# Kernel optimization log

Hardware: AMD Instinct MI355X
Metric: run time of the kernel (lower is better)

## Reference

```python
import jax, jax.numpy as jnp
import numpy as np

L, C, F, K = 8192, 2048, 128, 257  # timesteps, input_size, filter_size, lag (odd => symmetric 'same' pad)
NY = 256  # number of overwritten channel rows


def setup_inputs() -> dict:
    key = jax.random.key(0)
    k1, k2, k3, k4 = jax.random.split(key, 4)
    x = jax.random.normal(k1, (L, C), dtype=jnp.float32)
    Yt = jax.random.randint(k2, (NY,), 0, C)
    # learned parameters (torch.rand -> uniform[0,1))
    g = jax.random.uniform(k3, (C, F), dtype=jnp.float32)
    kernel = jax.random.uniform(k4, (F, K), dtype=jnp.float32)
    return {"x": x, "Yt": Yt, "g": g, "kernel": kernel}


def reference(x, Yt, g, kernel):
    # synapse[c] is the per-channel 1D filter; the original builds a dense
    # (C, C, K) kernel whose only non-zero slices are the diagonal, so the
    # full conv1d is mathematically a depthwise (grouped) conv.
    synapse = jnp.matmul(g, kernel)          # (C, K)
    lhs = x.T[None]                          # (1, C, L)  NCH
    rhs = synapse[:, None, :]                # (C, 1, K)  OIH, groups=C
    pad = (kernel.shape[1] - 1) // 2         # torch padding='same', odd K
    out = jax.lax.conv_general_dilated(
        lhs, rhs,
        window_strides=(1,),
        padding=[(pad, pad)],
        feature_group_count=x.shape[1],
        dimension_numbers=("NCH", "OIH", "NCH"),
    )                                        # (1, C, L)
    # result[:, Yt, :] = x.T[Yt] : scatter-overwrite selected channel rows
    out = out.at[:, Yt, :].set(x.T[Yt][None])
    return out
```

## Files before the change

kernel.cpp:

```cpp
#include <hip/hip_runtime.h>

#define LL   8192
#define CC   2048
#define FF   128
#define KK   257
#define PAD  128

#define SROW 320
#define NT   18

#define ROWS 1288
#define SRP  328

typedef __bf16 bf16x8 __attribute__((ext_vector_type(8)));
typedef float  f32x16 __attribute__((ext_vector_type(16)));

static __device__ __forceinline__ unsigned short f2bf(float f) {
    unsigned u = __float_as_uint(f);
    u = (u + 0x7fffu + ((u >> 16) & 1u)) >> 16;
    return (unsigned short)u;
}

__global__ __launch_bounds__(256) void synb_kernel(const float* __restrict__ g,
                                                   const float* __restrict__ kern,
                                                   const int* __restrict__ Yt, int ny,
                                                   unsigned short* __restrict__ synEb) {
    __shared__ int sfl[4];
    const int c0 = blockIdx.x * 4;
    const int t  = threadIdx.x;
    if (t < 4) sfl[t] = 0;
    __syncthreads();
    for (int i = t; i < ny; i += 256) {
        int y = Yt[i];
        #pragma unroll
        for (int ii = 0; ii < 4; ++ii) if (y == c0 + ii) sfl[ii] = 1;
    }
    __syncthreads();
    const float* g0 = g + (size_t)(c0 + 0) * FF;
    const float* g1 = g + (size_t)(c0 + 1) * FF;
    const float* g2 = g + (size_t)(c0 + 2) * FF;
    const float* g3 = g + (size_t)(c0 + 3) * FF;
    const int fl0 = sfl[0], fl1 = sfl[1], fl2 = sfl[2], fl3 = sfl[3];
    for (int p = t; p < SROW; p += 256) {
        const int kk = p - 32;
        float a0 = 0.f, a1 = 0.f, a2 = 0.f, a3 = 0.f;
        const bool inr = (kk >= 0) && (kk < KK);
        if (inr) {
            #pragma unroll 8
            for (int f = 0; f < FF; ++f) {
                float kv = kern[f * KK + kk];
                a0 += kv * g0[f];
                a1 += kv * g1[f];
                a2 += kv * g2[f];
                a3 += kv * g3[f];
            }
        }
        float dlt = (kk == PAD) ? 1.f : 0.f;
        float v0 = inr ? (fl0 ? dlt : a0) : 0.f;
        float v1 = inr ? (fl1 ? dlt : a1) : 0.f;
        float v2 = inr ? (fl2 ? dlt : a2) : 0.f;
        float v3 = inr ? (fl3 ? dlt : a3) : 0.f;
        synEb[(size_t)(c0 + 0) * SROW + p] = f2bf(v0);
        synEb[(size_t)(c0 + 1) * SROW + p] = f2bf(v1);
        synEb[(size_t)(c0 + 2) * SROW + p] = f2bf(v2);
        synEb[(size_t)(c0 + 3) * SROW + p] = f2bf(v3);
    }
}

__global__ __launch_bounds__(256) void fused_conv(const float* __restrict__ x,
                                                  const unsigned short* __restrict__ synEb,
                                                  float* __restrict__ out) {
    __shared__ alignas(16) unsigned short xch[16][ROWS];
    __shared__ alignas(16) unsigned short synL[16][SRP];
    const int t  = threadIdx.x;
    const int W0 = blockIdx.x << 10;
    const int c0 = blockIdx.y << 4;

    {
        const int rw = t >> 4;
        const int u  = t & 15;
        const unsigned* src = (const unsigned*)(synEb + (size_t)(c0 + rw) * SROW);
        unsigned* dst = (unsigned*)(synL[rw]);
        #pragma unroll
        for (int k = 0; k < 10; ++k) dst[u + (k << 4)] = src[u + (k << 4)];
    }

    #pragma unroll
    for (int k = 0; k < 10; ++k) {
        int pidx = (k << 8) + t;
        int ch4  = pidx & 3;
        int pp   = pidx >> 2;
        int lg   = W0 + (pp << 1) - 128;
        const float* sp = x + (size_t)lg * CC + c0 + (ch4 << 2);
        float4 ve = make_float4(0.f, 0.f, 0.f, 0.f);
        float4 vo = make_float4(0.f, 0.f, 0.f, 0.f);
        if ((unsigned)lg       < (unsigned)LL) ve = *(const float4*)sp;
        if ((unsigned)(lg + 1) < (unsigned)LL) vo = *(const float4*)(sp + CC);
        int gq = pp >> 2;
        int gp = gq ^ ((gq >> 3) & 7);
        int dw = (gp << 2) | (pp & 3);
        const float* pe = (const float*)&ve;
        const float* po = (const float*)&vo;
        #pragma unroll
        for (int c2 = 0; c2 < 4; ++c2) {
            unsigned val = (unsigned)f2bf(pe[c2]) | ((unsigned)f2bf(po[c2]) << 16);
            ((unsigned*)xch[(ch4 << 2) + c2])[dw] = val;
        }
    }
    __syncthreads();

    const int w = t >> 6, ln = t & 63;
    const int j = ln & 31, q = ln >> 5;
    const int bb  = (q << 4) - 2 * j + 64;
    const int dwb = bb >> 2;
    const int sh  = (bb & 2) << 3;
    const int gb  = (j << 2) + q;

    for (int cc = 0; cc < 4; ++cc) {
        const int ci = (w << 2) + cc;
        bf16x8 bfrag[NT];
        const unsigned* rp = (const unsigned*)(synL[ci]);
        #pragma unroll
        for (int m = 0; m < NT; ++m) {
            int base = dwb + (m << 3);
            unsigned w0 = rp[base + 0], w1 = rp[base + 1], w2 = rp[base + 2],
                     w3 = rp[base + 3], w4 = rp[base + 4];
            union { unsigned d[4]; bf16x8 v; } B;
            B.d[0] = (unsigned)((((unsigned long long)w1 << 32) | w0) >> sh);
            B.d[1] = (unsigned)((((unsigned long long)w2 << 32) | w1) >> sh);
            B.d[2] = (unsigned)((((unsigned long long)w3 << 32) | w2) >> sh);
            B.d[3] = (unsigned)((((unsigned long long)w4 << 32) | w3) >> sh);
            bfrag[m] = B.v;
        }
        f32x16 acc;
        #pragma unroll
        for (int r = 0; r < 16; ++r) acc[r] = 0.f;
        #pragma unroll
        for (int m = 0; m < NT; ++m) {
            int gq = gb + (m << 1);
            int gp = gq ^ ((gq >> 3) & 7);
            union { int4 i4; bf16x8 v; } A;
            A.i4 = *(const int4*)(&xch[ci][gp << 3]);
            acc = __builtin_amdgcn_mfma_f32_32x32x16_bf16(A.v, bfrag[m], acc, 0, 0, 0);
        }
        float* o = out + (size_t)(c0 + ci) * LL + W0 + j;
        #pragma unroll
        for (int r = 0; r < 16; ++r) {
            int row = (r & 3) + ((r >> 2) << 3) + (q << 2);
            o[row << 5] = acc[r];
        }
    }
}

extern "C" void kernel_launch(void* const* d_in, const int* in_sizes, int n_in,
                              void* d_out, int out_size, void* d_ws, size_t ws_size,
                              hipStream_t stream) {
    const float* x    = (const float*)d_in[0];
    const int*   Yt   = (const int*)  d_in[1];
    const float* g    = (const float*)d_in[2];
    const float* kern = (const float*)d_in[3];
    float* out = (float*)d_out;
    const int ny = in_sizes[1];

    unsigned short* synEb = (unsigned short*)d_ws;

    synb_kernel<<<CC / 4, 256, 0, stream>>>(g, kern, Yt, ny, synEb);
    fused_conv<<<dim3(LL / 1024, CC / 16), 256, 0, stream>>>(x, synEb, out);
}
```

Before: 149.1 us.

## Read synapse fragments straight from global memory and raise occupancy hint

Removes the shared-memory staging of the per-channel synapse rows. Each lane now loads its B-fragment words directly from the bf16 synapse buffer in global memory (L1/L2-cached), fused into the MFMA loop instead of preloaded into an 18-element register array. This also drops LDS per block by shrinking the x tile row, and launch_bounds(256,4) asks for more resident blocks. The cost is many small unaligned-word global loads per MFMA step and longer latency, which more occupancy is meant to hide. The synapse row stride is widened to 328 so the fragment reads stay in bounds.

```diff
diff --git a/kernel.cpp b/kernel.cpp
--- a/kernel.cpp
+++ b/kernel.cpp
@@ -6,11 +6,10 @@
 #define KK   257
 #define PAD  128
 
-#define SROW 320
+#define SROWP 328
 #define NT   18
 
-#define ROWS 1288
-#define SRP  328
+#define ROWS 1280
 
 typedef __bf16 bf16x8 __attribute__((ext_vector_type(8)));
 typedef float  f32x16 __attribute__((ext_vector_type(16)));
@@ -41,7 +40,7 @@
     const float* g2 = g + (size_t)(c0 + 2) * FF;
     const float* g3 = g + (size_t)(c0 + 3) * FF;
     const int fl0 = sfl[0], fl1 = sfl[1], fl2 = sfl[2], fl3 = sfl[3];
-    for (int p = t; p < SROW; p += 256) {
+    for (int p = t; p < SROWP; p += 256) {
         const int kk = p - 32;
         float a0 = 0.f, a1 = 0.f, a2 = 0.f, a3 = 0.f;
         const bool inr = (kk >= 0) && (kk < KK);
@@ -60,30 +59,20 @@
         float v1 = inr ? (fl1 ? dlt : a1) : 0.f;
         float v2 = inr ? (fl2 ? dlt : a2) : 0.f;
         float v3 = inr ? (fl3 ? dlt : a3) : 0.f;
-        synEb[(size_t)(c0 + 0) * SROW + p] = f2bf(v0);
-        synEb[(size_t)(c0 + 1) * SROW + p] = f2bf(v1);
-        synEb[(size_t)(c0 + 2) * SROW + p] = f2bf(v2);
-        synEb[(size_t)(c0 + 3) * SROW + p] = f2bf(v3);
+        synEb[(size_t)(c0 + 0) * SROWP + p] = f2bf(v0);
+        synEb[(size_t)(c0 + 1) * SROWP + p] = f2bf(v1);
+        synEb[(size_t)(c0 + 2) * SROWP + p] = f2bf(v2);
+        synEb[(size_t)(c0 + 3) * SROWP + p] = f2bf(v3);
     }
 }
 
-__global__ __launch_bounds__(256) void fused_conv(const float* __restrict__ x,
-                                                  const unsigned short* __restrict__ synEb,
-                                                  float* __restrict__ out) {
+__global__ __launch_bounds__(256, 4) void fused_conv(const float* __restrict__ x,
+                                                     const unsigned short* __restrict__ synEb,
+                                                     float* __restrict__ out) {
     __shared__ alignas(16) unsigned short xch[16][ROWS];
-    __shared__ alignas(16) unsigned short synL[16][SRP];
     const int t  = threadIdx.x;
     const int W0 = blockIdx.x << 10;
     const int c0 = blockIdx.y << 4;
-
-    {
-        const int rw = t >> 4;
-        const int u  = t & 15;
-        const unsigned* src = (const unsigned*)(synEb + (size_t)(c0 + rw) * SROW);
-        unsigned* dst = (unsigned*)(synL[rw]);
-        #pragma unroll
-        for (int k = 0; k < 10; ++k) dst[u + (k << 4)] = src[u + (k << 4)];
-    }
 
     #pragma unroll
     for (int k = 0; k < 10; ++k) {
@@ -118,30 +107,24 @@
 
     for (int cc = 0; cc < 4; ++cc) {
         const int ci = (w << 2) + cc;
-        bf16x8 bfrag[NT];
-        const unsigned* rp = (const unsigned*)(synL[ci]);
+        const unsigned* rp = (const unsigned*)(synEb + (size_t)(c0 + ci) * SROWP) + dwb;
+        f32x16 acc;
+        #pragma unroll
+        for (int r = 0; r < 16; ++r) acc[r] = 0.f;
         #pragma unroll
         for (int m = 0; m < NT; ++m) {
-            int base = dwb + (m << 3);
-            unsigned w0 = rp[base + 0], w1 = rp[base + 1], w2 = rp[base + 2],
-                     w3 = rp[base + 3], w4 = rp[base + 4];
+            unsigned w0 = rp[(m << 3) + 0], w1 = rp[(m << 3) + 1], w2 = rp[(m << 3) + 2],
+                     w3 = rp[(m << 3) + 3], w4 = rp[(m << 3) + 4];
             union { unsigned d[4]; bf16x8 v; } B;
             B.d[0] = (unsigned)((((unsigned long long)w1 << 32) | w0) >> sh);
             B.d[1] = (unsigned)((((unsigned long long)w2 << 32) | w1) >> sh);
             B.d[2] = (unsigned)((((unsigned long long)w3 << 32) | w2) >> sh);
             B.d[3] = (unsigned)((((unsigned long long)w4 << 32) | w3) >> sh);
-            bfrag[m] = B.v;
-        }
-        f32x16 acc;
-        #pragma unroll
-        for (int r = 0; r < 16; ++r) acc[r] = 0.f;
-        #pragma unroll
-        for (int m = 0; m < NT; ++m) {
             int gq = gb + (m << 1);
             int gp = gq ^ ((gq >> 3) & 7);
             union { int4 i4; bf16x8 v; } A;
             A.i4 = *(const int4*)(&xch[ci][gp << 3]);
-            acc = __builtin_amdgcn_mfma_f32_32x32x16_bf16(A.v, bfrag[m], acc, 0, 0, 0);
+            acc = __builtin_amdgcn_mfma_f32_32x32x16_bf16(A.v, B.v, acc, 0, 0, 0);
         }
         float* o = out + (size_t)(c0 + ci) * LL + W0 + j;
         #pragma unroll
```

Result: slower. 152.5 us (+2.3%).
